# Kernel optimization log

Measured on AMD Instinct MI355X. Metric: run time of the kernel, lower is better.

## Reference

```python
import jax, jax.numpy as jnp
import numpy as np

ALPHA = 0.2  # LeakyReLU negative slope (module init arg)


def setup_inputs() -> dict:
    key = jax.random.key(0)
    ks = jax.random.split(key, 5)
    b, w, K, E = 8, 256, 256, 512  # batch, window_size, n_features, embed (=2*window)
    x = jax.random.normal(ks[0], (b, w, K), dtype=jnp.float32)
    W = jax.random.normal(ks[1], (E, 2 * w), dtype=jnp.float32) * 0.05
    b_lin = jax.random.normal(ks[2], (E,), dtype=jnp.float32) * 0.05
    a = jax.random.normal(ks[3], (E,), dtype=jnp.float32) * 0.05
    bias = jax.random.normal(ks[4], (K, K), dtype=jnp.float32) * 0.05
    return {"x": x, "W": W, "b_lin": b_lin, "a": a, "bias": bias}


def reference(x, W, b_lin, a, bias):
    # x: (b, window, K) -> v: (b, K, window)
    v = jnp.transpose(x, (0, 2, 1))
    w = v.shape[2]
    # lin(concat(v_i, v_j)) == v_i @ Wl^T + v_j @ Wr^T + b_lin  (split weight)
    Wl, Wr = W[:, :w], W[:, w:]
    left = jnp.einsum('bkw,ew->bke', v, Wl)    # (b, K, E)
    right = jnp.einsum('bkw,ew->bke', v, Wr)   # (b, K, E)
    pre = left[:, :, None, :] + right[:, None, :, :] + b_lin  # (b, K, K, E)
    act = jax.nn.leaky_relu(pre, negative_slope=ALPHA)
    e = jnp.einsum('bije,e->bij', act, a) + bias               # (b, K, K)
    attn = jax.nn.softmax(e, axis=2)  # dropout p=0 in eval -> identity
    h = jax.nn.sigmoid(jnp.einsum('bij,bjw->biw', attn, v))    # (b, K, window)
    return jnp.transpose(h, (0, 2, 1))                          # (b, window, K)
```

## Files before the change

kernel.cpp:

```cpp
#include <hip/hip_runtime.h>
#include <math.h>

typedef float f32x4 __attribute__((ext_vector_type(4)));
typedef __bf16 bf16x8 __attribute__((ext_vector_type(8)));
typedef unsigned short u16x8 __attribute__((ext_vector_type(8)));

__device__ __forceinline__ unsigned short f2bf(float f) {
    union { float f; unsigned int u; } v; v.f = f;
    unsigned int u = v.u;
    return (unsigned short)((u + 0x7fffu + ((u >> 16) & 1u)) >> 16);
}
__device__ __forceinline__ float bf_lo(unsigned int d) {
    union { unsigned int u; float f; } v; v.u = d << 16; return v.f;
}
__device__ __forceinline__ float bf_hi(unsigned int d) {
    union { unsigned int u; float f; } v; v.u = d & 0xffff0000u; return v.f;
}
__device__ __forceinline__ float sigmoidf_(float v) {
    return 1.f / (1.f + __expf(-v));
}

__global__ __launch_bounds__(256) void mfma_gemm_kernel(
    const float* __restrict__ x,
    const float* __restrict__ W,
    const float* __restrict__ b_lin,
    float* __restrict__ Lp,
    unsigned short* __restrict__ R2)
{
    const int b = blockIdx.y;
    const int t = blockIdx.x;
    const bool left = (t < 32);
    int m0, n0;
    if (left) { m0 = (t >> 3) * 64; n0 = (t & 7) * 64; }
    else      { const int tt = t - 32; m0 = (tt >> 2) * 64; n0 = (tt & 3) * 64; }

    __shared__ unsigned short As[64][72];
    __shared__ unsigned short Bs[64][72];

    unsigned short (*Ts)[72] = left ? As : Bs;
    unsigned short (*Ds)[72] = left ? Bs : As;
    const int cbase = left ? m0 : n0;
    const int rbase = left ? n0 : m0;
    const int coff  = left ? 0 : 256;

    const int tid  = threadIdx.x;
    const int wv   = tid >> 6;
    const int lane = tid & 63;
    const int wy = wv >> 1, wx = wv & 1;
    const int lr = lane & 15;
    const int lk = lane >> 4;

    const float* xb = x + b * 65536;

    f32x4 acc[2][2];
    #pragma unroll
    for (int i = 0; i < 2; i++)
        #pragma unroll
        for (int jj = 0; jj < 2; jj++) acc[i][jj] = (f32x4){0.f, 0.f, 0.f, 0.f};

    const int wl = tid >> 4;
    const int kg = tid & 15;
    const int dr = tid >> 2;
    const int dc = (tid & 3) * 16;

    for (int k0 = 0; k0 < 256; k0 += 64) {
        #pragma unroll
        for (int p = 0; p < 4; p++) {
            const int w = wl + 16 * p;
            const float4 v = *(const float4*)(xb + (k0 + w) * 256 + cbase + kg * 4);
            Ts[kg * 4 + 0][w] = f2bf(v.x);
            Ts[kg * 4 + 1][w] = f2bf(v.y);
            Ts[kg * 4 + 2][w] = f2bf(v.z);
            Ts[kg * 4 + 3][w] = f2bf(v.w);
        }
        {
            const float* src = W + (rbase + dr) * 512 + coff + k0 + dc;
            const float4 v0 = *(const float4*)(src);
            const float4 v1 = *(const float4*)(src + 4);
            const float4 v2 = *(const float4*)(src + 8);
            const float4 v3 = *(const float4*)(src + 12);
            u16x8 o0, o1;
            o0[0] = f2bf(v0.x); o0[1] = f2bf(v0.y); o0[2] = f2bf(v0.z); o0[3] = f2bf(v0.w);
            o0[4] = f2bf(v1.x); o0[5] = f2bf(v1.y); o0[6] = f2bf(v1.z); o0[7] = f2bf(v1.w);
            o1[0] = f2bf(v2.x); o1[1] = f2bf(v2.y); o1[2] = f2bf(v2.z); o1[3] = f2bf(v2.w);
            o1[4] = f2bf(v3.x); o1[5] = f2bf(v3.y); o1[6] = f2bf(v3.z); o1[7] = f2bf(v3.w);
            *(u16x8*)&Ds[dr][dc]     = o0;
            *(u16x8*)&Ds[dr][dc + 8] = o1;
        }
        __syncthreads();
        #pragma unroll
        for (int kk = 0; kk < 64; kk += 32) {
            const bf16x8 a0 = *(const bf16x8*)&As[wy * 32 + lr][kk + lk * 8];
            const bf16x8 a1 = *(const bf16x8*)&As[wy * 32 + 16 + lr][kk + lk * 8];
            const bf16x8 b0 = *(const bf16x8*)&Bs[wx * 32 + lr][kk + lk * 8];
            const bf16x8 b1 = *(const bf16x8*)&Bs[wx * 32 + 16 + lr][kk + lk * 8];
            acc[0][0] = __builtin_amdgcn_mfma_f32_16x16x32_bf16(a0, b0, acc[0][0], 0, 0, 0);
            acc[0][1] = __builtin_amdgcn_mfma_f32_16x16x32_bf16(a0, b1, acc[0][1], 0, 0, 0);
            acc[1][0] = __builtin_amdgcn_mfma_f32_16x16x32_bf16(a1, b0, acc[1][0], 0, 0, 0);
            acc[1][1] = __builtin_amdgcn_mfma_f32_16x16x32_bf16(a1, b1, acc[1][1], 0, 0, 0);
        }
        __syncthreads();
    }

    if (left) {
        #pragma unroll
        for (int mi = 0; mi < 2; mi++) {
            #pragma unroll
            for (int ni = 0; ni < 2; ni++) {
                const int row = m0 + wy * 32 + mi * 16 + lk * 4;
                const int col = n0 + wx * 32 + ni * 16 + lr;
                const float bl = b_lin[col];
                #pragma unroll
                for (int r = 0; r < 4; r++)
                    Lp[b * 131072 + (row + r) * 512 + col] = acc[mi][ni][r] + bl;
            }
        }
    } else {
        unsigned short* R2b = R2 + b * 131072;
        #pragma unroll
        for (int mi = 0; mi < 2; mi++) {
            #pragma unroll
            for (int ni = 0; ni < 2; ni++) {
                const int row = m0 + wy * 32 + mi * 16 + lk * 4;
                const int col = n0 + wx * 32 + ni * 16 + lr;
                ushort4 o;
                o.x = f2bf(acc[mi][ni][0]);
                o.y = f2bf(acc[mi][ni][1]);
                o.z = f2bf(acc[mi][ni][2]);
                o.w = f2bf(acc[mi][ni][3]);
                *(ushort4*)(R2b + (row >> 3) * 2048 + col * 8 + (row & 7)) = o;
            }
        }
    }
}

__global__ __launch_bounds__(1024, 4) void attn_kernel(
    const float* __restrict__ x,
    const float* __restrict__ Lp,
    const unsigned int* __restrict__ R2u,
    const float* __restrict__ a,
    const float* __restrict__ bias,
    float* __restrict__ out)
{
    const int b   = blockIdx.x & 7;
    const int i0  = (blockIdx.x >> 3) * 8;
    const int tid = threadIdx.x;
    const int j   = tid & 255;
    const int q   = __builtin_amdgcn_readfirstlane(tid >> 8);

    __shared__ float acc2P[8192];
    __shared__ float rgp[1024];
    __shared__ float atf[2048];
    __shared__ float u15s[8];
    __shared__ unsigned short atbf[16 * 264];

    if (tid < 512) {
        const int i = tid >> 6, lane = tid & 63;
        const float* Lr = Lp + b * 131072 + (i0 + i) * 512 + lane * 8;
        const float* ar = a + lane * 8;
        const float4 la = *(const float4*)Lr;
        const float4 lb = *(const float4*)(Lr + 4);
        const float4 ca = *(const float4*)ar;
        const float4 cb = *(const float4*)(ar + 4);
        float p = la.x * ca.x + la.y * ca.y + la.z * ca.z + la.w * ca.w
                + lb.x * cb.x + lb.y * cb.y + lb.z * cb.z + lb.w * cb.w;
        #pragma unroll
        for (int off = 32; off; off >>= 1) p += __shfl_xor(p, off);
        if (lane == 0) u15s[i] = 0.6f * p;
    }

    const float* Lq = Lp + b * 131072 + i0 * 512 + q * 128;
    const float* aq = a + q * 128;
    const uint4* Rq = (const uint4*)(R2u + b * 65536) + q * 16 * 256 + j;

    float acc[8];
    #pragma unroll
    for (int i = 0; i < 8; i++) acc[i] = 0.f;
    float rsum = 0.f;

    for (int tk = 0; tk < 16; tk++) {
        const uint4 rw = Rq[tk * 256];
        float r[8];
        r[0] = bf_lo(rw.x); r[1] = bf_hi(rw.x);
        r[2] = bf_lo(rw.y); r[3] = bf_hi(rw.y);
        r[4] = bf_lo(rw.z); r[5] = bf_hi(rw.z);
        r[6] = bf_lo(rw.w); r[7] = bf_hi(rw.w);
        #pragma unroll
        for (int s = 0; s < 8; s++) {
            const int el = tk * 8 + s;
            const float ae = aq[el];
            rsum = fmaf(ae, r[s], rsum);
            #pragma unroll
            for (int i = 0; i < 8; i++) {
                const float p = Lq[i * 512 + el] + r[s];
                acc[i] = fmaf(ae, fabsf(p), acc[i]);
            }
        }
    }
    {
        float* dst = acc2P + q * 2048 + j;
        #pragma unroll
        for (int i = 0; i < 8; i++) dst[i * 256] = acc[i];
        rgp[q * 256 + j] = rsum;
    }
    __syncthreads();

    if (tid < 256) {
        const float uR = rgp[j] + rgp[256 + j] + rgp[512 + j] + rgp[768 + j];
        #pragma unroll
        for (int i = 0; i < 8; i++) {
            const float ab = acc2P[i * 256 + j] + acc2P[2048 + i * 256 + j]
                           + acc2P[4096 + i * 256 + j] + acc2P[6144 + i * 256 + j];
            atf[i * 256 + j] = u15s[i] + 0.6f * uR + 0.4f * ab
                             + bias[(i0 + i) * 256 + j];
        }
    }
    __syncthreads();

    if (tid < 512) {
        const int i = tid >> 6, lane = tid & 63;
        float v[4];
        float m = -1e30f;
        #pragma unroll
        for (int u = 0; u < 4; u++) {
            v[u] = atf[i * 256 + lane + 64 * u];
            m = fmaxf(m, v[u]);
        }
        #pragma unroll
        for (int off = 32; off; off >>= 1) m = fmaxf(m, __shfl_xor(m, off));
        float s = 0.f;
        #pragma unroll
        for (int u = 0; u < 4; u++) { v[u] = __expf(v[u] - m); s += v[u]; }
        #pragma unroll
        for (int off = 32; off; off >>= 1) s += __shfl_xor(s, off);
        const float inv = 1.f / s;
        #pragma unroll
        for (int u = 0; u < 4; u++)
            atbf[i * 264 + lane + 64 * u] = f2bf(v[u] * inv);
    }
    __syncthreads();

    {
        const int nt = tid >> 6;
        const int lane = tid & 63;
        const int lr = lane & 15;
        const int lk = lane >> 4;
        f32x4 hacc = (f32x4){0.f, 0.f, 0.f, 0.f};
        const float* xw = x + b * 65536 + (nt * 16 + lr) * 256;
        #pragma unroll
        for (int kt = 0; kt < 8; kt++) {
            const bf16x8 av = *(const bf16x8*)&atbf[lr * 264 + kt * 32 + lk * 8];
            const float4 f0 = *(const float4*)(xw + kt * 32 + lk * 8);
            const float4 f1 = *(const float4*)(xw + kt * 32 + lk * 8 + 4);
            u16x8 bu;
            bu[0] = f2bf(f0.x); bu[1] = f2bf(f0.y); bu[2] = f2bf(f0.z); bu[3] = f2bf(f0.w);
            bu[4] = f2bf(f1.x); bu[5] = f2bf(f1.y); bu[6] = f2bf(f1.z); bu[7] = f2bf(f1.w);
            const bf16x8 bv = *(const bf16x8*)&bu;
            hacc = __builtin_amdgcn_mfma_f32_16x16x32_bf16(av, bv, hacc, 0, 0, 0);
        }
        if (lk < 2) {
            float4 o;
            o.x = sigmoidf_(hacc[0]);
            o.y = sigmoidf_(hacc[1]);
            o.z = sigmoidf_(hacc[2]);
            o.w = sigmoidf_(hacc[3]);
            *(float4*)(out + b * 65536 + (nt * 16 + lr) * 256 + i0 + lk * 4) = o;
        }
    }
}

extern "C" void kernel_launch(void* const* d_in, const int* in_sizes, int n_in,
                              void* d_out, int out_size, void* d_ws, size_t ws_size,
                              hipStream_t stream) {
    const float* x     = (const float*)d_in[0];
    const float* W     = (const float*)d_in[1];
    const float* b_lin = (const float*)d_in[2];
    const float* a     = (const float*)d_in[3];
    const float* bias  = (const float*)d_in[4];
    float* out = (float*)d_out;

    char* ws = (char*)d_ws;
    float*          Lp = (float*)ws;
    unsigned short* R2 = (unsigned short*)(ws + (4 << 20));

    mfma_gemm_kernel<<<dim3(64, 8), 256, 0, stream>>>(x, W, b_lin, Lp, R2);
    attn_kernel<<<256, 1024, 0, stream>>>(x, Lp, (const unsigned int*)R2, a, bias, out);
}
```

Before: 116.5 us.

## Halve rows per attention block, double grid, and prefetch R tiles

Each attention block now handles 4 query rows instead of 8, and the grid doubles to 512 blocks so more CUs are busy. The inner loop software-prefetches the next R tile into registers, and the unused rows of the bf16 attention tile are zero-filled before the MFMA stage. In exchange, the R tiles are read twice as often in total and per-block fixed costs such as the x load for the final matmul are repeated across more blocks.

```diff
diff --git a/kernel.cpp b/kernel.cpp
--- a/kernel.cpp
+++ b/kernel.cpp
@@ -143,18 +143,18 @@
     float* __restrict__ out)
 {
     const int b   = blockIdx.x & 7;
-    const int i0  = (blockIdx.x >> 3) * 8;
+    const int i0  = (blockIdx.x >> 3) * 4;
     const int tid = threadIdx.x;
     const int j   = tid & 255;
     const int q   = __builtin_amdgcn_readfirstlane(tid >> 8);
 
-    __shared__ float acc2P[8192];
+    __shared__ float acc2P[4096];
     __shared__ float rgp[1024];
-    __shared__ float atf[2048];
-    __shared__ float u15s[8];
+    __shared__ float atf[1024];
+    __shared__ float u15s[4];
     __shared__ unsigned short atbf[16 * 264];
 
-    if (tid < 512) {
+    if (tid < 256) {
         const int i = tid >> 6, lane = tid & 63;
         const float* Lr = Lp + b * 131072 + (i0 + i) * 512 + lane * 8;
         const float* ar = a + lane * 8;
@@ -171,53 +171,62 @@
 
     const float* Lq = Lp + b * 131072 + i0 * 512 + q * 128;
     const float* aq = a + q * 128;
-    const uint4* Rq = (const uint4*)(R2u + b * 65536) + q * 16 * 256 + j;
-
-    float acc[8];
-    #pragma unroll
-    for (int i = 0; i < 8; i++) acc[i] = 0.f;
-    float rsum = 0.f;
-
+    const uint4* Rq = (const uint4*)(R2u + b * 65536) + (q * 16) * 256 + j;
+
+    float acc0 = 0.f, acc1 = 0.f, acc2 = 0.f, acc3 = 0.f, rsum = 0.f;
+
+    uint4 cur = Rq[0];
+    #pragma unroll 2
     for (int tk = 0; tk < 16; tk++) {
-        const uint4 rw = Rq[tk * 256];
+        uint4 nxt;
+        if (tk < 15) nxt = Rq[(tk + 1) * 256];
         float r[8];
-        r[0] = bf_lo(rw.x); r[1] = bf_hi(rw.x);
-        r[2] = bf_lo(rw.y); r[3] = bf_hi(rw.y);
-        r[4] = bf_lo(rw.z); r[5] = bf_hi(rw.z);
-        r[6] = bf_lo(rw.w); r[7] = bf_hi(rw.w);
+        r[0] = bf_lo(cur.x); r[1] = bf_hi(cur.x);
+        r[2] = bf_lo(cur.y); r[3] = bf_hi(cur.y);
+        r[4] = bf_lo(cur.z); r[5] = bf_hi(cur.z);
+        r[6] = bf_lo(cur.w); r[7] = bf_hi(cur.w);
         #pragma unroll
         for (int s = 0; s < 8; s++) {
             const int el = tk * 8 + s;
             const float ae = aq[el];
             rsum = fmaf(ae, r[s], rsum);
-            #pragma unroll
-            for (int i = 0; i < 8; i++) {
-                const float p = Lq[i * 512 + el] + r[s];
-                acc[i] = fmaf(ae, fabsf(p), acc[i]);
-            }
-        }
+            const float p0 = Lq[el]        + r[s];
+            const float p1 = Lq[512 + el]  + r[s];
+            const float p2 = Lq[1024 + el] + r[s];
+            const float p3 = Lq[1536 + el] + r[s];
+            acc0 = fmaf(ae, fabsf(p0), acc0);
+            acc1 = fmaf(ae, fabsf(p1), acc1);
+            acc2 = fmaf(ae, fabsf(p2), acc2);
+            acc3 = fmaf(ae, fabsf(p3), acc3);
+        }
+        cur = nxt;
     }
     {
-        float* dst = acc2P + q * 2048 + j;
-        #pragma unroll
-        for (int i = 0; i < 8; i++) dst[i * 256] = acc[i];
+        float* dst = acc2P + q * 1024 + j;
+        dst[0]   = acc0;
+        dst[256] = acc1;
+        dst[512] = acc2;
+        dst[768] = acc3;
         rgp[q * 256 + j] = rsum;
+    }
+    if (tid >= 512 && tid < 768) {
+        for (int z = tid - 512; z < 12 * 264; z += 256) atbf[4 * 264 + z] = 0;
     }
     __syncthreads();
 
     if (tid < 256) {
         const float uR = rgp[j] + rgp[256 + j] + rgp[512 + j] + rgp[768 + j];
         #pragma unroll
-        for (int i = 0; i < 8; i++) {
-            const float ab = acc2P[i * 256 + j] + acc2P[2048 + i * 256 + j]
-                           + acc2P[4096 + i * 256 + j] + acc2P[6144 + i * 256 + j];
+        for (int i = 0; i < 4; i++) {
+            const float ab = acc2P[i * 256 + j] + acc2P[1024 + i * 256 + j]
+                           + acc2P[2048 + i * 256 + j] + acc2P[3072 + i * 256 + j];
             atf[i * 256 + j] = u15s[i] + 0.6f * uR + 0.4f * ab
                              + bias[(i0 + i) * 256 + j];
         }
     }
     __syncthreads();
 
-    if (tid < 512) {
+    if (tid < 256) {
         const int i = tid >> 6, lane = tid & 63;
         float v[4];
         float m = -1e30f;
@@ -258,13 +267,13 @@
             const bf16x8 bv = *(const bf16x8*)&bu;
             hacc = __builtin_amdgcn_mfma_f32_16x16x32_bf16(av, bv, hacc, 0, 0, 0);
         }
-        if (lk < 2) {
+        if (lk == 0) {
             float4 o;
             o.x = sigmoidf_(hacc[0]);
             o.y = sigmoidf_(hacc[1]);
             o.z = sigmoidf_(hacc[2]);
             o.w = sigmoidf_(hacc[3]);
-            *(float4*)(out + b * 65536 + (nt * 16 + lr) * 256 + i0 + lk * 4) = o;
+            *(float4*)(out + b * 65536 + (nt * 16 + lr) * 256 + i0) = o;
         }
     }
 }
@@ -284,5 +293,5 @@
     unsigned short* R2 = (unsigned short*)(ws + (4 << 20));
 
     mfma_gemm_kernel<<<dim3(64, 8), 256, 0, stream>>>(x, W, b_lin, Lp, R2);
-    attn_kernel<<<256, 1024, 0, stream>>>(x, Lp, (const unsigned int*)R2, a, bias, out);
-}
+    attn_kernel<<<512, 1024, 0, stream>>>(x, Lp, (const unsigned int*)R2, a, bias, out);
+}
```

After: 123.3 us. 5.9% more time.
